# Optimization experiments

Hardware: AMD Instinct MI355X
Metric: run time of the kernel (lower is better)

The kernel has to match this reference:

```python
import jax, jax.numpy as jnp
import numpy as np

N_NODES = 100000
N_EDGES = 1600000
IN_FEATS = 128
OUT_FEATS = 128


def setup_inputs() -> dict:
    key = jax.random.key(0)
    k1, k2, k3, k4, k5 = jax.random.split(key, 5)
    feature = jax.random.normal(k1, (N_NODES, IN_FEATS), dtype=jnp.float32)
    src = jax.random.randint(k2, (N_EDGES,), 0, N_NODES, dtype=jnp.int64)
    dst = jax.random.randint(k3, (N_EDGES,), 0, N_NODES, dtype=jnp.int64)
    # nn.Linear default init: U(-1/sqrt(in), 1/sqrt(in)); randn scaled is fine for a numeric baseline
    bound = 1.0 / np.sqrt(IN_FEATS)
    W = jax.random.uniform(k4, (OUT_FEATS, IN_FEATS), dtype=jnp.float32, minval=-bound, maxval=bound)
    b = jax.random.uniform(k5, (OUT_FEATS,), dtype=jnp.float32, minval=-bound, maxval=bound)
    return {"feature": feature, "src": src, "dst": dst, "W": W, "b": b}


def reference(feature, src, dst, W, b):
    # message passing: copy source feature along each edge, sum into destination node
    agg = jax.ops.segment_sum(feature[src], dst, num_segments=N_NODES)  # [N, in_feats]
    # node apply: ReLU(Linear(h))
    return jax.nn.relu(agg @ W.T + b)  # [N, out_feats]
```

## Files before the change

### kernel.cpp

```cpp
#include <hip/hip_runtime.h>

#define N_NODES 100000
#define N_EDGES 1600000
#define F 128

#define NB    1563
#define NBP2  2048
#define CAP   1280
#define CHUNK 8192

#define BIN_BLOCKS  196
#define FEAT_BLOCKS 3125
#define WCONV_BLOCKS 16
#define FRONT_GRID  (BIN_BLOCKS + FEAT_BLOCKS + WCONV_BLOCKS)

typedef __bf16  bf16x8 __attribute__((ext_vector_type(8)));
typedef float   f32x4  __attribute__((ext_vector_type(4)));

__device__ inline unsigned short f32_to_bf16(float f) {
    unsigned u = __builtin_bit_cast(unsigned, f);
    u += 0x7FFFu + ((u >> 16) & 1u);
    return (unsigned short)(u >> 16);
}
__device__ inline unsigned pack_bf16x2(float lo, float hi) {
    return (unsigned)f32_to_bf16(lo) | ((unsigned)f32_to_bf16(hi) << 16);
}
__device__ inline void addrow(float* acc, const uint4 v) {
    acc[0] += __builtin_bit_cast(float, v.x << 16);
    acc[1] += __builtin_bit_cast(float, v.x & 0xFFFF0000u);
    acc[2] += __builtin_bit_cast(float, v.y << 16);
    acc[3] += __builtin_bit_cast(float, v.y & 0xFFFF0000u);
    acc[4] += __builtin_bit_cast(float, v.z << 16);
    acc[5] += __builtin_bit_cast(float, v.z & 0xFFFF0000u);
    acc[6] += __builtin_bit_cast(float, v.w << 16);
    acc[7] += __builtin_bit_cast(float, v.w & 0xFFFF0000u);
}

__global__ __launch_bounds__(1024) void gcn_front(
    const float* __restrict__ feat, const float* __restrict__ W,
    const int* __restrict__ src, const int* __restrict__ dst,
    int* __restrict__ gcur, unsigned* __restrict__ bins,
    unsigned short* __restrict__ Wbf, float* __restrict__ out)
{
    __shared__ unsigned cnt[NBP2];
    __shared__ unsigned off[NBP2];
    __shared__ int      gbase[NBP2];
    __shared__ unsigned staged[CHUNK];
    __shared__ unsigned short sbk[CHUNK];
    __shared__ unsigned scan[1024];

    const int tid = threadIdx.x;
    const int bx  = blockIdx.x;

    if (bx >= BIN_BLOCKS) {
        const int rb = bx - BIN_BLOCKS;
        if (rb < FEAT_BLOCKS) {
            const int t = rb * 1024 + tid;
            const float4 v = *(const float4*)(feat + (size_t)t * 4);
            uint2 p;
            p.x = pack_bf16x2(v.x, v.y);
            p.y = pack_bf16x2(v.z, v.w);
            const int n = t >> 5, q = t & 31;
            *(uint2*)((char*)out + (size_t)n * 512 + q * 8) = p;
        } else {
            const int i = (rb - FEAT_BLOCKS) * 1024 + tid;
            Wbf[i] = f32_to_bf16(W[i]);
        }
        return;
    }

    const int e0 = bx * CHUNK;

    #pragma unroll
    for (int i = 0; i < 2; ++i) cnt[tid + i * 1024] = 0;
    __syncthreads();

    int sv[8], dv[8];
    #pragma unroll
    for (int i = 0; i < 8; ++i) {
        const int e = e0 + tid + i * 1024;
        if (e < N_EDGES) {
            sv[i] = src[e];
            dv[i] = dst[e];
            atomicAdd(&cnt[dv[i] >> 6], 1u);
        } else dv[i] = -1;
    }
    __syncthreads();

    const unsigned s = cnt[2 * tid] + cnt[2 * tid + 1];
    scan[tid] = s;
    __syncthreads();
    for (int o = 1; o < 1024; o <<= 1) {
        const unsigned t = (tid >= o) ? scan[tid - o] : 0;
        __syncthreads();
        scan[tid] += t;
        __syncthreads();
    }
    const unsigned run = scan[tid] - s;
    off[2 * tid]     = run;
    off[2 * tid + 1] = run + cnt[2 * tid];
    __syncthreads();

    #pragma unroll
    for (int i = 0; i < 8; ++i) {
        if (dv[i] >= 0) {
            const int bk = dv[i] >> 6;
            const unsigned w = (unsigned)sv[i] | ((unsigned)(dv[i] & 63) << 17);
            const unsigned p = atomicAdd(&off[bk], 1u);
            staged[p] = w;
            sbk[p] = (unsigned short)bk;
        }
    }
    __syncthreads();

    #pragma unroll
    for (int i = 0; i < 2; ++i) {
        const int bk = 2 * tid + i;
        if (bk < NB && cnt[bk] > 0)
            gbase[bk] = atomicAdd(&gcur[bk], (int)cnt[bk]);
    }
    __syncthreads();

    const int c_tot = (int)scan[1023];
    for (int p = tid; p < c_tot; p += 1024) {
        const int bk = sbk[p];
        const int gp = gbase[bk] + (p - (int)(off[bk] - cnt[bk]));
        if (gp < CAP) bins[(size_t)bk * CAP + gp] = staged[p];
    }
}

__global__ __launch_bounds__(512) void gcn_accum2(
    const int* __restrict__ gcur,
    const unsigned* __restrict__ bins,
    float* __restrict__ out)
{
    __shared__ unsigned tmp[CAP];
    __shared__ unsigned list[CAP];
    __shared__ int cnt64[64], scn[64], pos64[64], cur64[64];

    const int tid = threadIdx.x;
    const int bkt = blockIdx.x;

    int c = gcur[bkt]; if (c > CAP) c = CAP;
    const unsigned* bb = bins + (size_t)bkt * CAP;

    for (int i = tid; i < c; i += 512) tmp[i] = bb[i];
    if (tid < 64) cnt64[tid] = 0;
    __syncthreads();

    for (int i = tid; i < c; i += 512) atomicAdd(&cnt64[(tmp[i] >> 17) & 63], 1);
    __syncthreads();

    if (tid < 64) scn[tid] = cnt64[tid];
    __syncthreads();
    #pragma unroll
    for (int o = 1; o < 64; o <<= 1) {
        int t = 0;
        if (tid < 64 && tid >= o) t = scn[tid - o];
        __syncthreads();
        if (tid < 64) scn[tid] += t;
        __syncthreads();
    }
    if (tid < 64) {
        const int st = scn[tid] - cnt64[tid];
        pos64[tid] = st;
        cur64[tid] = st;
    }
    __syncthreads();

    for (int i = tid; i < c; i += 512) {
        const unsigned w = tmp[i];
        const int p = atomicAdd(&cur64[(w >> 17) & 63], 1);
        list[p] = w;
    }
    __syncthreads();

    const int grp = tid >> 4;
    const int sl  = tid & 15;
    const int n0  = bkt * 64;

    #pragma unroll
    for (int ni = 0; ni < 2; ++ni) {
        const int l  = grp * 2 + ni;
        const int st = pos64[l];
        const int en = st + cnt64[l];

        float a0[8] = {0,0,0,0,0,0,0,0};
        float a1[8] = {0,0,0,0,0,0,0,0};
        int k = st;
        for (; k + 3 < en; k += 4) {
            const unsigned w0 = list[k],     w1 = list[k + 1];
            const unsigned w2 = list[k + 2], w3 = list[k + 3];
            const uint4 v0 = *(const uint4*)((const char*)out + (size_t)(w0 & 0x1FFFF) * 512 + sl * 16);
            const uint4 v1 = *(const uint4*)((const char*)out + (size_t)(w1 & 0x1FFFF) * 512 + sl * 16);
            const uint4 v2 = *(const uint4*)((const char*)out + (size_t)(w2 & 0x1FFFF) * 512 + sl * 16);
            const uint4 v3 = *(const uint4*)((const char*)out + (size_t)(w3 & 0x1FFFF) * 512 + sl * 16);
            addrow(a0, v0); addrow(a1, v1); addrow(a0, v2); addrow(a1, v3);
        }
        for (; k < en; ++k) {
            const unsigned w0 = list[k];
            const uint4 v0 = *(const uint4*)((const char*)out + (size_t)(w0 & 0x1FFFF) * 512 + sl * 16);
            addrow(a0, v0);
        }
        #pragma unroll
        for (int q = 0; q < 8; ++q) a0[q] += a1[q];

        const int n = n0 + l;
        if (n < N_NODES) {
            uint4 o;
            o.x = pack_bf16x2(a0[0], a0[1]);
            o.y = pack_bf16x2(a0[2], a0[3]);
            o.z = pack_bf16x2(a0[4], a0[5]);
            o.w = pack_bf16x2(a0[6], a0[7]);
            *(uint4*)((char*)out + (size_t)n * 512 + 256 + sl * 16) = o;
        }
    }
}

#define MT   128
#define LDP  136

__global__ __launch_bounds__(256) void gcn_gemm_mfma(
    float* __restrict__ out,
    const unsigned short* __restrict__ Wbf,
    const float* __restrict__ b)
{
    __shared__ unsigned short Alds[MT * LDP];
    __shared__ unsigned short Wlds[F * LDP];

    const int tid  = threadIdx.x;
    const int row0 = blockIdx.x * MT;

    #pragma unroll
    for (int i = 0; i < 8; ++i) {
        const int c = tid + i * 256;
        const int r = c >> 4, cc = c & 15;
        *(uint4*)&Wlds[r * LDP + cc * 8] = *(const uint4*)&Wbf[c * 8];
    }
    #pragma unroll
    for (int i = 0; i < 8; ++i) {
        const int c = tid + i * 256;
        const int r = c >> 4, cc = c & 15;
        int gr = row0 + r; if (gr > N_NODES - 1) gr = N_NODES - 1;
        const uint4 v = *(const uint4*)((const char*)out + (size_t)gr * 512 + 256 + cc * 16);
        *(uint4*)&Alds[r * LDP + cc * 8] = v;
    }
    __syncthreads();

    const int lane = tid & 63;
    const int wv   = tid >> 6;
    const int lr   = lane & 15;
    const int lq   = lane >> 4;

    f32x4 acc[2][8] = {};
    #pragma unroll
    for (int kk = 0; kk < 4; ++kk) {
        bf16x8 a[2], w[8];
        #pragma unroll
        for (int i = 0; i < 2; ++i)
            a[i] = __builtin_bit_cast(bf16x8,
                *(const uint4*)&Alds[(wv * 32 + i * 16 + lr) * LDP + kk * 32 + lq * 8]);
        #pragma unroll
        for (int n = 0; n < 8; ++n)
            w[n] = __builtin_bit_cast(bf16x8,
                *(const uint4*)&Wlds[(n * 16 + lr) * LDP + kk * 32 + lq * 8]);
        #pragma unroll
        for (int i = 0; i < 2; ++i)
            #pragma unroll
            for (int n = 0; n < 8; ++n)
                acc[i][n] = __builtin_amdgcn_mfma_f32_16x16x32_bf16(a[i], w[n], acc[i][n], 0, 0, 0);
    }

    float bias[8];
    #pragma unroll
    for (int n = 0; n < 8; ++n) bias[n] = b[n * 16 + lr];

    #pragma unroll
    for (int i = 0; i < 2; ++i) {
        const int rbase = wv * 32 + i * 16 + lq * 4;
        #pragma unroll
        for (int rg = 0; rg < 4; ++rg) {
            const int gr = row0 + rbase + rg;
            if (gr < N_NODES) {
                float* orow = out + (size_t)gr * F;
                #pragma unroll
                for (int n = 0; n < 8; ++n) {
                    const float v = acc[i][n][rg] + bias[n];
                    orow[n * 16 + lr] = v > 0.0f ? v : 0.0f;
                }
            }
        }
    }
}

__global__ __launch_bounds__(256) void gcn_scatter(
    const float* __restrict__ feat,
    const int* __restrict__ src, const int* __restrict__ dst,
    float* __restrict__ agg)
{
    const int sub  = threadIdx.x >> 5;
    const int lane = threadIdx.x & 31;
    const long long e = (long long)blockIdx.x * 8 + sub;
    if (e >= N_EDGES) return;
    const int s = src[e], d = dst[e];
    const float4 v = *(const float4*)(feat + (size_t)s * F + lane * 4);
    float* ar = agg + (size_t)d * F + lane * 4;
    unsafeAtomicAdd(ar + 0, v.x);
    unsafeAtomicAdd(ar + 1, v.y);
    unsafeAtomicAdd(ar + 2, v.z);
    unsafeAtomicAdd(ar + 3, v.w);
}

#define GR  64
#define LDW 132
__global__ __launch_bounds__(256) void gcn_gemm_relu(
    float* __restrict__ agg_out,
    const float* __restrict__ W, const float* __restrict__ b)
{
    __shared__ float Wl[F][LDW];
    __shared__ float At[GR][LDW];
    const int tid = threadIdx.x;
    const long long row0 = (long long)blockIdx.x * GR;
    #pragma unroll
    for (int i = 0; i < 64; ++i) {
        const int e = tid + i * 256;
        Wl[e >> 7][e & 127] = W[e];
    }
    #pragma unroll
    for (int i = 0; i < 32; ++i) {
        const int e = tid + i * 256;
        const int r = e >> 7, k2 = e & 127;
        const long long gr = row0 + r;
        At[r][k2] = (gr < N_NODES) ? agg_out[gr * F + k2] : 0.0f;
    }
    __syncthreads();
    const int tx = tid & 15, ty = tid >> 4, r0 = ty * 4;
    float acc[4][8];
    #pragma unroll
    for (int r = 0; r < 4; ++r)
        #pragma unroll
        for (int m = 0; m < 8; ++m) acc[r][m] = 0.0f;
    for (int k0 = 0; k0 < F; k0 += 4) {
        float4 a[4], w[8];
        #pragma unroll
        for (int r = 0; r < 4; ++r) a[r] = *(const float4*)&At[r0 + r][k0];
        #pragma unroll
        for (int m = 0; m < 8; ++m) w[m] = *(const float4*)&Wl[tx + 16 * m][k0];
        #pragma unroll
        for (int r = 0; r < 4; ++r)
            #pragma unroll
            for (int m = 0; m < 8; ++m)
                acc[r][m] += a[r].x * w[m].x + a[r].y * w[m].y
                           + a[r].z * w[m].z + a[r].w * w[m].w;
    }
    float bias[8];
    #pragma unroll
    for (int m = 0; m < 8; ++m) bias[m] = b[tx + 16 * m];
    __syncthreads();
    #pragma unroll
    for (int r = 0; r < 4; ++r) {
        const long long gr = row0 + r0 + r;
        if (gr < N_NODES) {
            float* orow = agg_out + gr * F;
            #pragma unroll
            for (int m = 0; m < 8; ++m) {
                const float v = acc[r][m] + bias[m];
                orow[tx + 16 * m] = v > 0.0f ? v : 0.0f;
            }
        }
    }
}

extern "C" void kernel_launch(void* const* d_in, const int* in_sizes, int n_in,
                              void* d_out, int out_size, void* d_ws, size_t ws_size,
                              hipStream_t stream) {
    const float* feat = (const float*)d_in[0];
    const int*   src  = (const int*)d_in[1];
    const int*   dst  = (const int*)d_in[2];
    const float* W    = (const float*)d_in[3];
    const float* b    = (const float*)d_in[4];
    float* out = (float*)d_out;

    const size_t ws_need = 1600u * 4 + (size_t)NB * CAP * 4 + (size_t)F * F * 2;

    if (ws_size >= ws_need) {
        int* gcur = (int*)d_ws;
        unsigned* bins = (unsigned*)(gcur + 1600);
        unsigned short* Wbf = (unsigned short*)(bins + (size_t)NB * CAP);

        hipMemsetAsync(gcur, 0, NB * sizeof(int), stream);
        gcn_front   <<<FRONT_GRID, 1024, 0, stream>>>(feat, W, src, dst, gcur, bins, Wbf, out);
        gcn_accum2  <<<NB, 512, 0, stream>>>(gcur, bins, out);
        gcn_gemm_mfma<<<(N_NODES + MT - 1) / MT, 256, 0, stream>>>(out, Wbf, b);
    } else {
        hipMemsetAsync(out, 0, (size_t)N_NODES * F * sizeof(float), stream);
        gcn_scatter<<<N_EDGES / 8, 256, 0, stream>>>(feat, src, dst, out);
        gcn_gemm_relu<<<(N_NODES + GR - 1) / GR, 256, 0, stream>>>(out, W, b);
    }
}
```

Baseline: 196.0 us.

## Fuse neighbor aggregation with MFMA GEMM and stage bf16 features in workspace

Adds a fused kernel that aggregates each 64-node bucket into shared memory as bf16 and immediately runs the 128x128 bf16 MFMA linear layer with bias and ReLU, writing the final fp32 output. The bf16 feature copy moves to a dense 256-byte-stride workspace buffer instead of being packed into the output array. This removes the third kernel launch and the round trip of aggregated rows through global memory, and halves the footprint of the gathered feature table. The cost is more shared memory per block (W tile plus A tile), which may lower occupancy in the gather phase, and the path only runs when the workspace is large enough.

```diff
diff --git a/kernel.cpp b/kernel.cpp
--- a/kernel.cpp
+++ b/kernel.cpp
@@ -13,6 +13,8 @@
 #define FEAT_BLOCKS 3125
 #define WCONV_BLOCKS 16
 #define FRONT_GRID  (BIN_BLOCKS + FEAT_BLOCKS + WCONV_BLOCKS)
+
+#define LDP  136
 
 typedef __bf16  bf16x8 __attribute__((ext_vector_type(8)));
 typedef float   f32x4  __attribute__((ext_vector_type(4)));
@@ -40,7 +42,8 @@
     const float* __restrict__ feat, const float* __restrict__ W,
     const int* __restrict__ src, const int* __restrict__ dst,
     int* __restrict__ gcur, unsigned* __restrict__ bins,
-    unsigned short* __restrict__ Wbf, float* __restrict__ out)
+    unsigned short* __restrict__ Wbf,
+    char* __restrict__ featdst, int fstride)
 {
     __shared__ unsigned cnt[NBP2];
     __shared__ unsigned off[NBP2];
@@ -61,7 +64,7 @@
             p.x = pack_bf16x2(v.x, v.y);
             p.y = pack_bf16x2(v.z, v.w);
             const int n = t >> 5, q = t & 31;
-            *(uint2*)((char*)out + (size_t)n * 512 + q * 8) = p;
+            *(uint2*)(featdst + (size_t)n * fstride + q * 8) = p;
         } else {
             const int i = (rb - FEAT_BLOCKS) * 1024 + tid;
             Wbf[i] = f32_to_bf16(W[i]);
@@ -126,6 +129,144 @@
         const int bk = sbk[p];
         const int gp = gbase[bk] + (p - (int)(off[bk] - cnt[bk]));
         if (gp < CAP) bins[(size_t)bk * CAP + gp] = staged[p];
+    }
+}
+
+__global__ __launch_bounds__(512) void gcn_accum_gemm(
+    const int* __restrict__ gcur,
+    const unsigned* __restrict__ bins,
+    const unsigned short* __restrict__ featbf,
+    const unsigned short* __restrict__ Wbf,
+    const float* __restrict__ b,
+    float* __restrict__ out)
+{
+    __shared__ unsigned tmp[CAP];
+    __shared__ unsigned list[CAP];
+    __shared__ int cnt64[64], scn[64], pos64[64], cur64[64];
+    __shared__ unsigned short Alds[64 * LDP];
+    __shared__ unsigned short Wlds[F * LDP];
+
+    const int tid = threadIdx.x;
+    const int bkt = blockIdx.x;
+
+    #pragma unroll
+    for (int i = 0; i < 4; ++i) {
+        const int c2 = tid + i * 512;
+        const int r = c2 >> 4, cc = c2 & 15;
+        *(uint4*)&Wlds[r * LDP + cc * 8] = *(const uint4*)&Wbf[c2 * 8];
+    }
+
+    int c = gcur[bkt]; if (c > CAP) c = CAP;
+    const unsigned* bb = bins + (size_t)bkt * CAP;
+
+    for (int i = tid; i < c; i += 512) tmp[i] = bb[i];
+    if (tid < 64) cnt64[tid] = 0;
+    __syncthreads();
+
+    for (int i = tid; i < c; i += 512) atomicAdd(&cnt64[(tmp[i] >> 17) & 63], 1);
+    __syncthreads();
+
+    if (tid < 64) scn[tid] = cnt64[tid];
+    __syncthreads();
+    #pragma unroll
+    for (int o = 1; o < 64; o <<= 1) {
+        int t = 0;
+        if (tid < 64 && tid >= o) t = scn[tid - o];
+        __syncthreads();
+        if (tid < 64) scn[tid] += t;
+        __syncthreads();
+    }
+    if (tid < 64) {
+        const int st = scn[tid] - cnt64[tid];
+        pos64[tid] = st;
+        cur64[tid] = st;
+    }
+    __syncthreads();
+
+    for (int i = tid; i < c; i += 512) {
+        const unsigned w = tmp[i];
+        const int p = atomicAdd(&cur64[(w >> 17) & 63], 1);
+        list[p] = w;
+    }
+    __syncthreads();
+
+    const int grp = tid >> 4;
+    const int sl  = tid & 15;
+    const int n0  = bkt * 64;
+
+    #pragma unroll
+    for (int ni = 0; ni < 2; ++ni) {
+        const int l  = grp * 2 + ni;
+        const int st = pos64[l];
+        const int en = st + cnt64[l];
+
+        float a0[8] = {0,0,0,0,0,0,0,0};
+        float a1[8] = {0,0,0,0,0,0,0,0};
+        int k = st;
+        for (; k + 3 < en; k += 4) {
+            const unsigned w0 = list[k],     w1 = list[k + 1];
+            const unsigned w2 = list[k + 2], w3 = list[k + 3];
+            const uint4 v0 = *(const uint4*)((const char*)featbf + (size_t)(w0 & 0x1FFFF) * 256 + sl * 16);
+            const uint4 v1 = *(const uint4*)((const char*)featbf + (size_t)(w1 & 0x1FFFF) * 256 + sl * 16);
+            const uint4 v2 = *(const uint4*)((const char*)featbf + (size_t)(w2 & 0x1FFFF) * 256 + sl * 16);
+            const uint4 v3 = *(const uint4*)((const char*)featbf + (size_t)(w3 & 0x1FFFF) * 256 + sl * 16);
+            addrow(a0, v0); addrow(a1, v1); addrow(a0, v2); addrow(a1, v3);
+        }
+        for (; k < en; ++k) {
+            const unsigned w0 = list[k];
+            const uint4 v0 = *(const uint4*)((const char*)featbf + (size_t)(w0 & 0x1FFFF) * 256 + sl * 16);
+            addrow(a0, v0);
+        }
+        #pragma unroll
+        for (int q = 0; q < 8; ++q) a0[q] += a1[q];
+
+        uint4 o;
+        o.x = pack_bf16x2(a0[0], a0[1]);
+        o.y = pack_bf16x2(a0[2], a0[3]);
+        o.z = pack_bf16x2(a0[4], a0[5]);
+        o.w = pack_bf16x2(a0[6], a0[7]);
+        *(uint4*)&Alds[l * LDP + sl * 8] = o;
+    }
+    __syncthreads();
+
+    const int lane = tid & 63;
+    const int wv   = tid >> 6;
+    const int lr   = lane & 15;
+    const int lq   = lane >> 4;
+    const int rf   = wv >> 1;
+    const int ch   = (wv & 1) * 4;
+
+    f32x4 acc[4] = {};
+    #pragma unroll
+    for (int kk = 0; kk < 4; ++kk) {
+        const bf16x8 a = __builtin_bit_cast(bf16x8,
+            *(const uint4*)&Alds[(rf * 16 + lr) * LDP + kk * 32 + lq * 8]);
+        bf16x8 w[4];
+        #pragma unroll
+        for (int n = 0; n < 4; ++n)
+            w[n] = __builtin_bit_cast(bf16x8,
+                *(const uint4*)&Wlds[((ch + n) * 16 + lr) * LDP + kk * 32 + lq * 8]);
+        #pragma unroll
+        for (int n = 0; n < 4; ++n)
+            acc[n] = __builtin_amdgcn_mfma_f32_16x16x32_bf16(a, w[n], acc[n], 0, 0, 0);
+    }
+
+    float bs[4];
+    #pragma unroll
+    for (int n = 0; n < 4; ++n) bs[n] = b[(ch + n) * 16 + lr];
+
+    #pragma unroll
+    for (int rg = 0; rg < 4; ++rg) {
+        const int row = rf * 16 + lq * 4 + rg;
+        const int gn  = n0 + row;
+        if (gn < N_NODES) {
+            float* orow = out + (size_t)gn * F;
+            #pragma unroll
+            for (int n = 0; n < 4; ++n) {
+                const float v = acc[n][rg] + bs[n];
+                orow[(ch + n) * 16 + lr] = v > 0.0f ? v : 0.0f;
+            }
+        }
     }
 }
 
@@ -147,10 +288,8 @@
     for (int i = tid; i < c; i += 512) tmp[i] = bb[i];
     if (tid < 64) cnt64[tid] = 0;
     __syncthreads();
-
     for (int i = tid; i < c; i += 512) atomicAdd(&cnt64[(tmp[i] >> 17) & 63], 1);
     __syncthreads();
-
     if (tid < 64) scn[tid] = cnt64[tid];
     __syncthreads();
     #pragma unroll
@@ -167,7 +306,6 @@
         cur64[tid] = st;
     }
     __syncthreads();
-
     for (int i = tid; i < c; i += 512) {
         const unsigned w = tmp[i];
         const int p = atomicAdd(&cur64[(w >> 17) & 63], 1);
@@ -175,16 +313,12 @@
     }
     __syncthreads();
 
-    const int grp = tid >> 4;
-    const int sl  = tid & 15;
-    const int n0  = bkt * 64;
-
+    const int grp = tid >> 4, sl = tid & 15, n0 = bkt * 64;
     #pragma unroll
     for (int ni = 0; ni < 2; ++ni) {
         const int l  = grp * 2 + ni;
         const int st = pos64[l];
         const int en = st + cnt64[l];
-
         float a0[8] = {0,0,0,0,0,0,0,0};
         float a1[8] = {0,0,0,0,0,0,0,0};
         int k = st;
@@ -204,7 +338,6 @@
         }
         #pragma unroll
         for (int q = 0; q < 8; ++q) a0[q] += a1[q];
-
         const int n = n0 + l;
         if (n < N_NODES) {
             uint4 o;
@@ -217,9 +350,7 @@
     }
 }
 
-#define MT   128
-#define LDP  136
-
+#define MT 128
 __global__ __launch_bounds__(256) void gcn_gemm_mfma(
     float* __restrict__ out,
     const unsigned short* __restrict__ Wbf,
@@ -381,17 +512,27 @@
     const float* b    = (const float*)d_in[4];
     float* out = (float*)d_out;
 
-    const size_t ws_need = 1600u * 4 + (size_t)NB * CAP * 4 + (size_t)F * F * 2;
-
-    if (ws_size >= ws_need) {
+    const size_t ws_base = 1600u * 4 + (size_t)NB * CAP * 4 + (size_t)F * F * 2;
+    const size_t ws_full = ws_base + (size_t)N_NODES * F * 2;
+
+    if (ws_size >= ws_base) {
         int* gcur = (int*)d_ws;
         unsigned* bins = (unsigned*)(gcur + 1600);
         unsigned short* Wbf = (unsigned short*)(bins + (size_t)NB * CAP);
+        unsigned short* featbf = Wbf + (size_t)F * F;
 
         hipMemsetAsync(gcur, 0, NB * sizeof(int), stream);
-        gcn_front   <<<FRONT_GRID, 1024, 0, stream>>>(feat, W, src, dst, gcur, bins, Wbf, out);
-        gcn_accum2  <<<NB, 512, 0, stream>>>(gcur, bins, out);
-        gcn_gemm_mfma<<<(N_NODES + MT - 1) / MT, 256, 0, stream>>>(out, Wbf, b);
+
+        if (ws_size >= ws_full) {
+            gcn_front<<<FRONT_GRID, 1024, 0, stream>>>(
+                feat, W, src, dst, gcur, bins, Wbf, (char*)featbf, 256);
+            gcn_accum_gemm<<<NB, 512, 0, stream>>>(gcur, bins, featbf, Wbf, b, out);
+        } else {
+            gcn_front<<<FRONT_GRID, 1024, 0, stream>>>(
+                feat, W, src, dst, gcur, bins, Wbf, (char*)out, 512);
+            gcn_accum2<<<NB, 512, 0, stream>>>(gcur, bins, out);
+            gcn_gemm_mfma<<<(N_NODES + MT - 1) / MT, 256, 0, stream>>>(out, Wbf, b);
+        }
     } else {
         hipMemsetAsync(out, 0, (size_t)N_NODES * F * sizeof(float), stream);
         gcn_scatter<<<N_EDGES / 8, 256, 0, stream>>>(feat, src, dst, out);
```

New measurement: 196.0 us. About the same (+0.0%).
